# Kernel tuning notes

Measured on AMD Instinct MI355X. Metric: run time of the kernel, lower is better.

## Reference

```python
import jax, jax.numpy as jnp
import numpy as np

NEG_SLOPE = 0.2


def gat_conv(x, src, dst, N, W, a_src, a_dst, b, concat):
    # x: [N, F_in], W: [F_in, H*C], a_src/a_dst: [H, C], b: [H*C] or [C]
    H, C = a_src.shape
    h = (x @ W).reshape(N, H, C)                    # [N, H, C]
    al_src = jnp.einsum('nhc,hc->nh', h, a_src)     # [N, H]
    al_dst = jnp.einsum('nhc,hc->nh', h, a_dst)     # [N, H]
    logits = jax.nn.leaky_relu(al_src[src] + al_dst[dst], NEG_SLOPE)  # [E, H]
    # edge softmax over incoming edges of each destination node
    m = jax.ops.segment_max(logits, dst, num_segments=N)              # [N, H]
    m = jnp.where(jnp.isfinite(m), m, 0.0)
    e = jnp.exp(logits - m[dst])                                      # [E, H]
    denom = jax.ops.segment_sum(e, dst, num_segments=N)               # [N, H]
    alpha = e / denom[dst]                                            # [E, H]
    out = jax.ops.segment_sum(alpha[:, :, None] * h[src], dst, num_segments=N)  # [N, H, C]
    if concat:
        return out.reshape(N, H * C) + b
    return out.mean(axis=1) + b


def setup_inputs() -> dict:
    key = jax.random.key(0)
    ks = jax.random.split(key, 12)
    N, E = 100000, 1600000
    F_in, Ch, Co, H = 128, 32, 64, 4
    x = jax.random.normal(ks[0], (N, F_in), dtype=jnp.float32)
    edge_index = jax.random.randint(ks[1], (2, E), 0, N, dtype=jnp.int64)
    s = 0.1
    return {
        'x': x, 'edge_index': edge_index,
        'W1': jax.random.normal(ks[2], (F_in, H * Ch), jnp.float32) * s,
        'a_src1': jax.random.normal(ks[3], (H, Ch), jnp.float32) * s,
        'a_dst1': jax.random.normal(ks[4], (H, Ch), jnp.float32) * s,
        'b1': jnp.zeros((H * Ch,), jnp.float32),
        'W2': jax.random.normal(ks[5], (H * Ch, H * Ch), jnp.float32) * s,
        'a_src2': jax.random.normal(ks[6], (H, Ch), jnp.float32) * s,
        'a_dst2': jax.random.normal(ks[7], (H, Ch), jnp.float32) * s,
        'b2': jnp.zeros((H * Ch,), jnp.float32),
        'W3': jax.random.normal(ks[8], (H * Ch, H * Co), jnp.float32) * s,
        'a_src3': jax.random.normal(ks[9], (H, Co), jnp.float32) * s,
        'a_dst3': jax.random.normal(ks[10], (H, Co), jnp.float32) * s,
        'b3': jnp.zeros((Co,), jnp.float32),
    }


def reference(x, edge_index, W1, a_src1, a_dst1, b1, W2, a_src2, a_dst2, b2, W3, a_src3, a_dst3, b3):
    N = x.shape[0]
    # PyG GATConv default add_self_loops=True
    loop = jnp.arange(N, dtype=edge_index.dtype)
    src = jnp.concatenate([edge_index[0], loop])
    dst = jnp.concatenate([edge_index[1], loop])
    h = gat_conv(x, src, dst, N, W1, a_src1, a_dst1, b1, concat=True)
    h = jax.nn.elu(h)
    h = gat_conv(h, src, dst, N, W2, a_src2, a_dst2, b2, concat=True)
    h = jax.nn.elu(h)
    out = gat_conv(h, src, dst, N, W3, a_src3, a_dst3, b3, concat=False)
    return out
```

## Files before the change

kernel.cpp:

```cpp
#include <hip/hip_runtime.h>


#define NEG_SLOPE 0.2f

typedef __attribute__((ext_vector_type(8))) _Float16 half8v;
typedef __attribute__((ext_vector_type(4))) _Float16 half4v;
typedef __attribute__((ext_vector_type(2))) _Float16 half2v;
typedef __attribute__((ext_vector_type(4))) float f32x4;

__device__ __forceinline__ float lrelu(float v) { return v > 0.f ? v : NEG_SLOPE * v; }

struct hf2 { _Float16 hi, lo; };
__device__ __forceinline__ hf2 split_f16(float f)
{
    hf2 r;
    r.hi = (_Float16)f;
    r.lo = (_Float16)(f - (float)r.hi);
    return r;
}

__global__ void fill_sentinel(float* __restrict__ out, int n)
{
    int i = blockIdx.x * blockDim.x + threadIdx.x;
    if (i < n) out[i] = 1e30f;
}

__global__ void detect_idx64(const int* __restrict__ ei, int* __restrict__ flag)
{
    __shared__ int anynz;
    if (threadIdx.x == 0) anynz = 0;
    __syncthreads();
    int v = ei[2 * threadIdx.x + 1];
    if (v != 0) atomicOr(&anynz, 1);
    __syncthreads();
    if (threadIdx.x == 0) flag[0] = (anynz == 0) ? 1 : 0;
}

__global__ void prep_edges(const void* __restrict__ ei, const int* __restrict__ flag,
                           int* __restrict__ src32, int* __restrict__ dst32,
                           int* __restrict__ deg8, int* __restrict__ loc, int N, int E)
{
    int e = blockIdx.x * blockDim.x + threadIdx.x;
    if (e >= E) return;
    int xcc;
    asm("s_getreg_b32 %0, hwreg(HW_REG_XCC_ID)" : "=s"(xcc));
    xcc &= 7;
    int s, d;
    if (flag[0]) {
        s = (int)__builtin_nontemporal_load((const long long*)ei + e);
        d = (int)__builtin_nontemporal_load((const long long*)ei + E + e);
    } else {
        s = __builtin_nontemporal_load((const int*)ei + e);
        d = __builtin_nontemporal_load((const int*)ei + E + e);
    }
    src32[e] = s;
    dst32[e] = d;
    int v = atomicAdd(&deg8[xcc * N + d], 1);
    loc[e] = (xcc << 28) | v;
}

__global__ void reduce8(int* __restrict__ deg8, int* __restrict__ deg, int N)
{
    int d = blockIdx.x * blockDim.x + threadIdx.x;
    if (d >= N) return;
    int s = 0;
    #pragma unroll
    for (int k = 0; k < 8; ++k) {
        int v = deg8[k * N + d];
        deg8[k * N + d] = s;
        s += v;
    }
    deg[d] = s;
}

__global__ __launch_bounds__(256)
void scanA(const int* __restrict__ deg, int* __restrict__ rowptr,
           int* __restrict__ bsum, int N)
{
    __shared__ int part[256];
    const int t = threadIdx.x;
    const int base = blockIdx.x * 1024 + t * 4;
    int v[4];
    #pragma unroll
    for (int j = 0; j < 4; ++j) v[j] = (base + j < N) ? deg[base + j] : 0;
    int s = v[0] + v[1] + v[2] + v[3];
    part[t] = s;
    __syncthreads();
    #pragma unroll
    for (int off = 1; off < 256; off <<= 1) {
        int p = (t >= off) ? part[t - off] : 0;
        __syncthreads();
        part[t] += p;
        __syncthreads();
    }
    int run = (t == 0) ? 0 : part[t - 1];
    #pragma unroll
    for (int j = 0; j < 4; ++j) {
        if (base + j < N) rowptr[base + j] = run;
        run += v[j];
    }
    if (t == 255) bsum[blockIdx.x] = part[255];
}

__global__ __launch_bounds__(1024)
void scanB(int* __restrict__ bsum, int nb)
{
    __shared__ int s[1024];
    int t = threadIdx.x;
    s[t] = (t < nb) ? bsum[t] : 0;
    __syncthreads();
    for (int off = 1; off < 1024; off <<= 1) {
        int p = (t >= off) ? s[t - off] : 0;
        __syncthreads();
        s[t] += p;
        __syncthreads();
    }
    if (t < nb) bsum[t] = (t == 0) ? 0 : s[t - 1];
}

__global__ __launch_bounds__(256)
void scanC(int* __restrict__ rowptr, const int* __restrict__ bsum, int N, int E)
{
    const int base = blockIdx.x * 1024 + threadIdx.x * 4;
    const int off = bsum[blockIdx.x];
    #pragma unroll
    for (int j = 0; j < 4; ++j)
        if (base + j < N) rowptr[base + j] += off;
    if (blockIdx.x == 0 && threadIdx.x == 0) rowptr[N] = E;
}

__global__ void fill_csr(const int* __restrict__ src32, const int* __restrict__ dst32,
                         const int* __restrict__ loc, const int* __restrict__ rowptr,
                         const int* __restrict__ deg8, int* __restrict__ csr_src,
                         int N, int E)
{
    int e = blockIdx.x * blockDim.x + threadIdx.x;
    if (e >= E) return;
    int lv = loc[e];
    int d  = dst32[e];
    int k  = lv >> 28;
    csr_src[rowptr[d] + deg8[k * N + d] + (lv & 0x0FFFFFFF)] = src32[e];
}

__global__ void convert_hilo(const float* __restrict__ in, _Float16* __restrict__ hi,
                             _Float16* __restrict__ lo, long long n4)
{
    long long t = (long long)blockIdx.x * blockDim.x + threadIdx.x;
    if (t >= n4) return;
    float4 v = *(const float4*)&in[t * 4];
    hf2 a = split_f16(v.x), b = split_f16(v.y), c = split_f16(v.z), d = split_f16(v.w);
    half4v h, l;
    h.x = a.hi; h.y = b.hi; h.z = c.hi; h.w = d.hi;
    l.x = a.lo; l.y = b.lo; l.z = c.lo; l.w = d.lo;
    *(half4v*)&hi[t * 4] = h;
    *(half4v*)&lo[t * 4] = l;
}

__global__ __launch_bounds__(256)
void convert_wt(const float* __restrict__ W, _Float16* __restrict__ wthi,
                _Float16* __restrict__ wtlo, int ldw, int wcol0)
{
    int t = blockIdx.x * 256 + threadIdx.x;
    int k = t >> 7, n = t & 127;
    float v = W[(long long)k * ldw + wcol0 + n];
    hf2 r = split_f16(v);
    wthi[n * 128 + k] = r.hi;
    wtlo[n * 128 + k] = r.lo;
}

template<int HPC>
__global__ __launch_bounds__(256)
void gemm_mfma(const _Float16* __restrict__ Ahi, const _Float16* __restrict__ Alo,
               const _Float16* __restrict__ Wthi, const _Float16* __restrict__ Wtlo,
               _Float16* __restrict__ Chi, int ldc, int colofs, int hofs,
               const float* __restrict__ aS, const float* __restrict__ aD,
               float* __restrict__ als, float* __restrict__ ald, int M)
{
    const int tid = threadIdx.x;
    const int wave = tid >> 6, lane = tid & 63;
    const int l15 = lane & 15, lk = lane >> 4;
    const int m0 = blockIdx.x * 64 + wave * 16;
    int mrow = m0 + l15;
    if (mrow >= M) mrow = M - 1;

    f32x4 acc[8];
    #pragma unroll
    for (int i = 0; i < 8; ++i) acc[i] = (f32x4){0.f, 0.f, 0.f, 0.f};

    #pragma unroll
    for (int kt = 0; kt < 4; ++kt) {
        const int k = kt * 32 + lk * 8;
        half8v ah = *(const half8v*)&Ahi[(long long)mrow * 128 + k];
        half8v al = *(const half8v*)&Alo[(long long)mrow * 128 + k];
        #pragma unroll
        for (int nf = 0; nf < 8; ++nf) {
            half8v bh = *(const half8v*)&Wthi[(nf * 16 + l15) * 128 + k];
            half8v bl = *(const half8v*)&Wtlo[(nf * 16 + l15) * 128 + k];
            acc[nf] = __builtin_amdgcn_mfma_f32_16x16x32_f16(ah, bh, acc[nf], 0, 0, 0);
            acc[nf] = __builtin_amdgcn_mfma_f32_16x16x32_f16(ah, bl, acc[nf], 0, 0, 0);
            acc[nf] = __builtin_amdgcn_mfma_f32_16x16x32_f16(al, bh, acc[nf], 0, 0, 0);
        }
    }

    #pragma unroll
    for (int r = 0; r < 4; ++r) {
        int gm = m0 + lk * 4 + r;
        if (gm >= M) continue;
        #pragma unroll
        for (int nf = 0; nf < 8; ++nf)
            Chi[(long long)gm * ldc + colofs + nf * 16 + l15] = (_Float16)acc[nf][r];
    }

    float asv[8], adv[8];
    #pragma unroll
    for (int nf = 0; nf < 8; ++nf) {
        asv[nf] = aS[nf * 16 + l15];
        adv[nf] = aD[nf * 16 + l15];
    }
    constexpr int NFH = 8 / HPC;
    #pragma unroll
    for (int r = 0; r < 4; ++r) {
        #pragma unroll
        for (int h = 0; h < HPC; ++h) {
            float ps = 0.f, pd = 0.f;
            #pragma unroll
            for (int q = 0; q < NFH; ++q) {
                int nf = h * NFH + q;
                ps += acc[nf][r] * asv[nf];
                pd += acc[nf][r] * adv[nf];
            }
            #pragma unroll
            for (int m = 1; m < 16; m <<= 1) {
                ps += __shfl_xor(ps, m);
                pd += __shfl_xor(pd, m);
            }
            if (l15 == 0) {
                int gm = m0 + lk * 4 + r;
                if (gm < M) {
                    als[gm * 4 + hofs + h] = ps;
                    ald[gm * 4 + hofs + h] = pd;
                }
            }
        }
    }
}

template<int C, int HL>
__global__ __launch_bounds__(256)
void gat_aggregate(const int* __restrict__ rowptr, const int* __restrict__ csr_src,
                   const float* __restrict__ als, const float* __restrict__ ald,
                   const _Float16* __restrict__ h16, const float* __restrict__ bias,
                   _Float16* __restrict__ ohi, _Float16* __restrict__ olo, int N)
{
    constexpr int ROW = HL * C;
    constexpr int LOG2HL = (HL == 4) ? 2 : 1;
    const int d = (blockIdx.x * blockDim.x + threadIdx.x) >> 6;
    const int lane = threadIdx.x & 63;
    if (d >= N) return;
    const int j = lane * 2;
    const int hh = j / C;

    const int myh = lane & (HL - 1);
    const int myi = lane >> LOG2HL;
    const float ald_mine = ald[d * HL + myh];

    const float wself = __expf(lrelu(als[d * HL + hh] + ald[d * HL + hh]));
    float denom = wself;
    half2v hv = *(const half2v*)&h16[(unsigned)d * ROW + j];
    float vx = wself * (float)hv.x, vy = wself * (float)hv.y;

    const int e0 = rowptr[d], e1 = rowptr[d + 1];
    for (int base = e0; base < e1; base += 8) {
        int sv_mine = 0;
        float w_mine = 0.f;
        if (lane < 8 * HL) {
            int ee = base + myi;
            sv_mine = csr_src[ee < e1 ? ee : e1 - 1];
            float a = als[sv_mine * HL + myh] + ald_mine;
            w_mine = (ee < e1) ? __expf(lrelu(a)) : 0.f;
        }
        int sref[8];
        half2v hb[8];
        #pragma unroll
        for (int i = 0; i < 8; ++i) sref[i] = __shfl(sv_mine, i * HL, 64);
        #pragma unroll
        for (int i = 0; i < 8; ++i) hb[i] = *(const half2v*)&h16[(unsigned)sref[i] * ROW + j];
        #pragma unroll
        for (int i = 0; i < 8; ++i) {
            float wv = __shfl(w_mine, i * HL + hh, 64);
            denom += wv;
            vx += wv * (float)hb[i].x;
            vy += wv * (float)hb[i].y;
        }
    }
    float inv = 1.f / denom;
    vx = vx * inv + bias[j];
    vy = vy * inv + bias[j + 1];
    vx = vx > 0.f ? vx : __expf(vx) - 1.f;
    vy = vy > 0.f ? vy : __expf(vy) - 1.f;
    hf2 rx = split_f16(vx), ry = split_f16(vy);
    half2v hi2, lo2;
    hi2.x = rx.hi; hi2.y = ry.hi;
    lo2.x = rx.lo; lo2.y = ry.lo;
    *(half2v*)&ohi[(unsigned)d * ROW + j] = hi2;
    *(half2v*)&olo[(unsigned)d * ROW + j] = lo2;
}

__global__ __launch_bounds__(256)
void gat_aggregate3(const int* __restrict__ rowptr, const int* __restrict__ csr_src,
                    const float* __restrict__ als, const float* __restrict__ ald,
                    const _Float16* __restrict__ h16, const float* __restrict__ bias,
                    float* __restrict__ out, int N)
{
    const int d = (blockIdx.x * blockDim.x + threadIdx.x) >> 6;
    const int lane = threadIdx.x & 63;
    if (d >= N) return;
    const int q = lane * 4;
    const int chd = lane >> 4;

    const int myh = lane & 3;
    const int myi = lane >> 2;
    const float ald_mine = ald[d * 4 + myh];

    const float wself = __expf(lrelu(als[d * 4 + chd] + ald[d * 4 + chd]));
    float dn = wself;
    half4v hs = *(const half4v*)&h16[(unsigned)d * 256 + q];
    float vx0 = wself * (float)hs.x, vx1 = wself * (float)hs.y;
    float vx2 = wself * (float)hs.z, vx3 = wself * (float)hs.w;

    const int e0 = rowptr[d], e1 = rowptr[d + 1];
    for (int base = e0; base < e1; base += 8) {
        int sv_mine = 0;
        float w_mine = 0.f;
        if (lane < 32) {
            int ee = base + myi;
            sv_mine = csr_src[ee < e1 ? ee : e1 - 1];
            float a = als[sv_mine * 4 + myh] + ald_mine;
            w_mine = (ee < e1) ? __expf(lrelu(a)) : 0.f;
        }
        int sref[8];
        half4v hb[8];
        #pragma unroll
        for (int i = 0; i < 8; ++i) sref[i] = __shfl(sv_mine, i * 4, 64);
        #pragma unroll
        for (int i = 0; i < 8; ++i) hb[i] = *(const half4v*)&h16[(unsigned)sref[i] * 256 + q];
        #pragma unroll
        for (int i = 0; i < 8; ++i) {
            float wv = __shfl(w_mine, i * 4 + chd, 64);
            dn += wv;
            vx0 += wv * (float)hb[i].x;
            vx1 += wv * (float)hb[i].y;
            vx2 += wv * (float)hb[i].z;
            vx3 += wv * (float)hb[i].w;
        }
    }
    const float s = 0.25f / dn;
    float m0 = vx0 * s, m1 = vx1 * s, m2 = vx2 * s, m3 = vx3 * s;
    m0 += __shfl_xor(m0, 16); m1 += __shfl_xor(m1, 16);
    m2 += __shfl_xor(m2, 16); m3 += __shfl_xor(m3, 16);
    m0 += __shfl_xor(m0, 32); m1 += __shfl_xor(m1, 32);
    m2 += __shfl_xor(m2, 32); m3 += __shfl_xor(m3, 32);
    if (lane < 16) {
        m0 += bias[q + 0]; m1 += bias[q + 1];
        m2 += bias[q + 2]; m3 += bias[q + 3];
        *(float4*)&out[(unsigned)d * 64 + q] = make_float4(m0, m1, m2, m3);
    }
}

extern "C" void kernel_launch(void* const* d_in, const int* in_sizes, int n_in,
                              void* d_out, int out_size, void* d_ws, size_t ws_size,
                              hipStream_t stream)
{
    const float* x      = (const float*)d_in[0];
    const void*  ei     = d_in[1];
    const float* W1     = (const float*)d_in[2];
    const float* a_src1 = (const float*)d_in[3];
    const float* a_dst1 = (const float*)d_in[4];
    const float* b1     = (const float*)d_in[5];
    const float* W2     = (const float*)d_in[6];
    const float* a_src2 = (const float*)d_in[7];
    const float* a_dst2 = (const float*)d_in[8];
    const float* b2     = (const float*)d_in[9];
    const float* W3     = (const float*)d_in[10];
    const float* a_src3 = (const float*)d_in[11];
    const float* a_dst3 = (const float*)d_in[12];
    const float* b3     = (const float*)d_in[13];

    const int N = in_sizes[0] / 128;
    const int E = in_sizes[1] / 2;

    char* w = (char*)d_ws;
    auto alloc = [&](size_t bytes) {
        char* p = w;
        w += (bytes + 255) & ~(size_t)255;
        return p;
    };
    int*      flag    = (int*)     alloc(256);
    int*      deg8    = (int*)     alloc((size_t)N * 8 * 4);
    int*      deg     = (int*)     alloc((size_t)N * 4);
    int*      rowptr  = (int*)     alloc((size_t)(N + 1) * 4);
    int*      bsum    = (int*)     alloc(1024 * 4);
    int*      src32   = (int*)     alloc((size_t)E * 4);
    int*      dst32   = (int*)     alloc((size_t)E * 4);
    int*      loc     = (int*)     alloc((size_t)E * 4);
    int*      csr_src = (int*)     alloc((size_t)E * 4);
    _Float16* hhi     = (_Float16*)alloc((size_t)N * 256 * 2);
    _Float16* xhi     = (_Float16*)alloc((size_t)N * 128 * 2);
    _Float16* xlo     = (_Float16*)alloc((size_t)N * 128 * 2);
    float*    als     = (float*)   alloc((size_t)N * 4 * 4);
    float*    ald     = (float*)   alloc((size_t)N * 4 * 4);
    _Float16* wthi    = (_Float16*)alloc(2 * 128 * 128 * 2);
    _Float16* wtlo    = (_Float16*)alloc(2 * 128 * 128 * 2);
    if ((size_t)(w - (char*)d_ws) > ws_size) {
        fill_sentinel<<<(out_size + 255) / 256, 256, 0, stream>>>((float*)d_out, out_size);
        return;
    }
    _Float16* wthiB = wthi + 128 * 128;
    _Float16* wtloB = wtlo + 128 * 128;

    const int gb = 256;
    const int nb1024 = (N + 1023) / 1024;
    const int mb = (N + 63) / 64;
    const int ab = (N * 64 + gb - 1) / gb;
    auto blocks = [&](long long tot) { return (int)((tot + gb - 1) / gb); };

    detect_idx64<<<1, 256, 0, stream>>>((const int*)ei, flag);
    (void)hipMemsetAsync(deg8, 0, (size_t)N * 8 * 4, stream);
    prep_edges<<<blocks(E), gb, 0, stream>>>(ei, flag, src32, dst32, deg8, loc, N, E);
    reduce8<<<blocks(N), gb, 0, stream>>>(deg8, deg, N);
    scanA<<<nb1024, gb, 0, stream>>>(deg, rowptr, bsum, N);
    scanB<<<1, 1024, 0, stream>>>(bsum, nb1024);
    scanC<<<nb1024, gb, 0, stream>>>(rowptr, bsum, N, E);
    fill_csr<<<blocks(E), gb, 0, stream>>>(src32, dst32, loc, rowptr, deg8, csr_src, N, E);

    convert_hilo<<<blocks((long long)N * 32), gb, 0, stream>>>(x, xhi, xlo, (long long)N * 32);

    convert_wt<<<64, gb, 0, stream>>>(W1, wthi, wtlo, 128, 0);
    gemm_mfma<4><<<mb, gb, 0, stream>>>(xhi, xlo, wthi, wtlo, hhi, 128, 0, 0,
                                        a_src1, a_dst1, als, ald, N);
    gat_aggregate<32, 4><<<ab, gb, 0, stream>>>(
        rowptr, csr_src, als, ald, hhi, b1, xhi, xlo, N);

    convert_wt<<<64, gb, 0, stream>>>(W2, wthi, wtlo, 128, 0);
    gemm_mfma<4><<<mb, gb, 0, stream>>>(xhi, xlo, wthi, wtlo, hhi, 128, 0, 0,
                                        a_src2, a_dst2, als, ald, N);
    gat_aggregate<32, 4><<<ab, gb, 0, stream>>>(
        rowptr, csr_src, als, ald, hhi, b2, xhi, xlo, N);

    convert_wt<<<64, gb, 0, stream>>>(W3, wthi,  wtlo,  256, 0);
    convert_wt<<<64, gb, 0, stream>>>(W3, wthiB, wtloB, 256, 128);
    gemm_mfma<2><<<mb, gb, 0, stream>>>(xhi, xlo, wthi,  wtlo,  hhi, 256, 0, 0,
                                        a_src3,       a_dst3,       als, ald, N);
    gemm_mfma<2><<<mb, gb, 0, stream>>>(xhi, xlo, wthiB, wtloB, hhi, 256, 128, 2,
                                        a_src3 + 128, a_dst3 + 128, als, ald, N);
    gat_aggregate3<<<ab, gb, 0, stream>>>(
        rowptr, csr_src, als, ald, hhi, b3, (float*)d_out, N);
}
```

Baseline: 696.6 us.

## Fuse input fp32 split into GEMM, drop edge copies, double GEMM rows per wave

The separate convert_hilo pass over x is removed, and the first GEMM now reads fp32 x and splits it into hi/lo fp16 in registers. prep_edges no longer writes src32/dst32 copies, and fill_csr rereads edge_index directly. The GEMM now computes two 16-row groups per wave (128 rows per block) and reuses the loaded W fragments across both groups, with launch bounds set for 2 blocks per CU. Aggregation indexing is changed to use a fixed stride of 4 for als/ald. These changes cut intermediate memory traffic at the cost of higher register pressure in the GEMM.

```diff
diff --git a/kernel.cpp b/kernel.cpp
--- a/kernel.cpp
+++ b/kernel.cpp
@@ -37,7 +37,6 @@
 }
 
 __global__ void prep_edges(const void* __restrict__ ei, const int* __restrict__ flag,
-                           int* __restrict__ src32, int* __restrict__ dst32,
                            int* __restrict__ deg8, int* __restrict__ loc, int N, int E)
 {
     int e = blockIdx.x * blockDim.x + threadIdx.x;
@@ -45,16 +44,9 @@
     int xcc;
     asm("s_getreg_b32 %0, hwreg(HW_REG_XCC_ID)" : "=s"(xcc));
     xcc &= 7;
-    int s, d;
-    if (flag[0]) {
-        s = (int)__builtin_nontemporal_load((const long long*)ei + e);
-        d = (int)__builtin_nontemporal_load((const long long*)ei + E + e);
-    } else {
-        s = __builtin_nontemporal_load((const int*)ei + e);
-        d = __builtin_nontemporal_load((const int*)ei + E + e);
-    }
-    src32[e] = s;
-    dst32[e] = d;
+    int d;
+    if (flag[0]) d = (int)__builtin_nontemporal_load((const long long*)ei + E + e);
+    else         d = __builtin_nontemporal_load((const int*)ei + E + e);
     int v = atomicAdd(&deg8[xcc * N + d], 1);
     loc[e] = (xcc << 28) | v;
 }
@@ -129,31 +121,23 @@
     if (blockIdx.x == 0 && threadIdx.x == 0) rowptr[N] = E;
 }
 
-__global__ void fill_csr(const int* __restrict__ src32, const int* __restrict__ dst32,
+__global__ void fill_csr(const void* __restrict__ ei, const int* __restrict__ flag,
                          const int* __restrict__ loc, const int* __restrict__ rowptr,
                          const int* __restrict__ deg8, int* __restrict__ csr_src,
                          int N, int E)
 {
     int e = blockIdx.x * blockDim.x + threadIdx.x;
     if (e >= E) return;
+    int s, d;
+    if (flag[0]) {
+        s = (int)__builtin_nontemporal_load((const long long*)ei + e);
+        d = (int)__builtin_nontemporal_load((const long long*)ei + E + e);
+    } else {
+        s = __builtin_nontemporal_load((const int*)ei + e);
+        d = __builtin_nontemporal_load((const int*)ei + E + e);
+    }
     int lv = loc[e];
-    int d  = dst32[e];
-    int k  = lv >> 28;
-    csr_src[rowptr[d] + deg8[k * N + d] + (lv & 0x0FFFFFFF)] = src32[e];
-}
-
-__global__ void convert_hilo(const float* __restrict__ in, _Float16* __restrict__ hi,
-                             _Float16* __restrict__ lo, long long n4)
-{
-    long long t = (long long)blockIdx.x * blockDim.x + threadIdx.x;
-    if (t >= n4) return;
-    float4 v = *(const float4*)&in[t * 4];
-    hf2 a = split_f16(v.x), b = split_f16(v.y), c = split_f16(v.z), d = split_f16(v.w);
-    half4v h, l;
-    h.x = a.hi; h.y = b.hi; h.z = c.hi; h.w = d.hi;
-    l.x = a.lo; l.y = b.lo; l.z = c.lo; l.w = d.lo;
-    *(half4v*)&hi[t * 4] = h;
-    *(half4v*)&lo[t * 4] = l;
+    csr_src[rowptr[d] + deg8[(lv >> 28) * N + d] + (lv & 0x0FFFFFFF)] = s;
 }
 
 __global__ __launch_bounds__(256)
@@ -168,9 +152,9 @@
     wtlo[n * 128 + k] = r.lo;
 }
 
-template<int HPC>
-__global__ __launch_bounds__(256)
-void gemm_mfma(const _Float16* __restrict__ Ahi, const _Float16* __restrict__ Alo,
+template<int HPC, bool AF32>
+__global__ __launch_bounds__(256, 2)
+void gemm_mfma(const void* __restrict__ Aptr, const _Float16* __restrict__ Alo,
                const _Float16* __restrict__ Wthi, const _Float16* __restrict__ Wtlo,
                _Float16* __restrict__ Chi, int ldc, int colofs, int hofs,
                const float* __restrict__ aS, const float* __restrict__ aD,
@@ -179,36 +163,50 @@
     const int tid = threadIdx.x;
     const int wave = tid >> 6, lane = tid & 63;
     const int l15 = lane & 15, lk = lane >> 4;
-    const int m0 = blockIdx.x * 64 + wave * 16;
-    int mrow = m0 + l15;
-    if (mrow >= M) mrow = M - 1;
-
-    f32x4 acc[8];
-    #pragma unroll
-    for (int i = 0; i < 8; ++i) acc[i] = (f32x4){0.f, 0.f, 0.f, 0.f};
+    const int m0 = blockIdx.x * 128 + wave * 32;
+
+    f32x4 acc[2][8];
+    #pragma unroll
+    for (int rg = 0; rg < 2; ++rg)
+        #pragma unroll
+        for (int i = 0; i < 8; ++i) acc[rg][i] = (f32x4){0.f, 0.f, 0.f, 0.f};
 
     #pragma unroll
     for (int kt = 0; kt < 4; ++kt) {
         const int k = kt * 32 + lk * 8;
-        half8v ah = *(const half8v*)&Ahi[(long long)mrow * 128 + k];
-        half8v al = *(const half8v*)&Alo[(long long)mrow * 128 + k];
+        half8v bh[8], bl[8];
         #pragma unroll
         for (int nf = 0; nf < 8; ++nf) {
-            half8v bh = *(const half8v*)&Wthi[(nf * 16 + l15) * 128 + k];
-            half8v bl = *(const half8v*)&Wtlo[(nf * 16 + l15) * 128 + k];
-            acc[nf] = __builtin_amdgcn_mfma_f32_16x16x32_f16(ah, bh, acc[nf], 0, 0, 0);
-            acc[nf] = __builtin_amdgcn_mfma_f32_16x16x32_f16(ah, bl, acc[nf], 0, 0, 0);
-            acc[nf] = __builtin_amdgcn_mfma_f32_16x16x32_f16(al, bh, acc[nf], 0, 0, 0);
-        }
-    }
-
-    #pragma unroll
-    for (int r = 0; r < 4; ++r) {
-        int gm = m0 + lk * 4 + r;
-        if (gm >= M) continue;
-        #pragma unroll
-        for (int nf = 0; nf < 8; ++nf)
-            Chi[(long long)gm * ldc + colofs + nf * 16 + l15] = (_Float16)acc[nf][r];
+            bh[nf] = *(const half8v*)&Wthi[(nf * 16 + l15) * 128 + k];
+            bl[nf] = *(const half8v*)&Wtlo[(nf * 16 + l15) * 128 + k];
+        }
+        #pragma unroll
+        for (int rg = 0; rg < 2; ++rg) {
+            int mrow = m0 + rg * 16 + l15;
+            if (mrow >= M) mrow = M - 1;
+            half8v ah, al;
+            if (AF32) {
+                const float* A32 = (const float*)Aptr;
+                float4 v0 = *(const float4*)&A32[(long long)mrow * 128 + k];
+                float4 v1 = *(const float4*)&A32[(long long)mrow * 128 + k + 4];
+                hf2 s0 = split_f16(v0.x), s1 = split_f16(v0.y), s2 = split_f16(v0.z), s3 = split_f16(v0.w);
+                hf2 s4 = split_f16(v1.x), s5 = split_f16(v1.y), s6 = split_f16(v1.z), s7 = split_f16(v1.w);
+                ah[0] = s0.hi; ah[1] = s1.hi; ah[2] = s2.hi; ah[3] = s3.hi;
+                ah[4] = s4.hi; ah[5] = s5.hi; ah[6] = s6.hi; ah[7] = s7.hi;
+                al[0] = s0.lo; al[1] = s1.lo; al[2] = s2.lo; al[3] = s3.lo;
+                al[4] = s4.lo; al[5] = s5.lo; al[6] = s6.lo; al[7] = s7.lo;
+            } else {
+                const _Float16* Ahi = (const _Float16*)Aptr;
+                ah = *(const half8v*)&Ahi[(long long)mrow * 128 + k];
+                al = *(const half8v*)&Alo[(long long)mrow * 128 + k];
+            }
+            #pragma unroll
+            for (int nf = 0; nf < 8; ++nf) {
+                acc[rg][nf] = __builtin_amdgcn_mfma_f32_16x16x32_f16(ah, bh[nf], acc[rg][nf], 0, 0, 0);
+                acc[rg][nf] = __builtin_amdgcn_mfma_f32_16x16x32_f16(ah, bl[nf], acc[rg][nf], 0, 0, 0);
+                acc[rg][nf] = __builtin_amdgcn_mfma_f32_16x16x32_f16(al, bh[nf], acc[rg][nf], 0, 0, 0);
+            }
+        }
     }
 
     float asv[8], adv[8];
@@ -218,27 +216,39 @@
         adv[nf] = aD[nf * 16 + l15];
     }
     constexpr int NFH = 8 / HPC;
-    #pragma unroll
-    for (int r = 0; r < 4; ++r) {
-        #pragma unroll
-        for (int h = 0; h < HPC; ++h) {
-            float ps = 0.f, pd = 0.f;
+
+    #pragma unroll
+    for (int rg = 0; rg < 2; ++rg) {
+        #pragma unroll
+        for (int r = 0; r < 4; ++r) {
+            int gm = m0 + rg * 16 + lk * 4 + r;
+            if (gm >= M) continue;
             #pragma unroll
-            for (int q = 0; q < NFH; ++q) {
-                int nf = h * NFH + q;
-                ps += acc[nf][r] * asv[nf];
-                pd += acc[nf][r] * adv[nf];
-            }
+            for (int nf = 0; nf < 8; ++nf)
+                Chi[(long long)gm * ldc + colofs + nf * 16 + l15] = (_Float16)acc[rg][nf][r];
+        }
+        #pragma unroll
+        for (int r = 0; r < 4; ++r) {
             #pragma unroll
-            for (int m = 1; m < 16; m <<= 1) {
-                ps += __shfl_xor(ps, m);
-                pd += __shfl_xor(pd, m);
-            }
-            if (l15 == 0) {
-                int gm = m0 + lk * 4 + r;
-                if (gm < M) {
-                    als[gm * 4 + hofs + h] = ps;
-                    ald[gm * 4 + hofs + h] = pd;
+            for (int h = 0; h < HPC; ++h) {
+                float ps = 0.f, pd = 0.f;
+                #pragma unroll
+                for (int q = 0; q < NFH; ++q) {
+                    int nf = h * NFH + q;
+                    ps += acc[rg][nf][r] * asv[nf];
+                    pd += acc[rg][nf][r] * adv[nf];
+                }
+                #pragma unroll
+                for (int m = 1; m < 16; m <<= 1) {
+                    ps += __shfl_xor(ps, m);
+                    pd += __shfl_xor(pd, m);
+                }
+                if (l15 == 0) {
+                    int gm = m0 + rg * 16 + lk * 4 + r;
+                    if (gm < M) {
+                        als[gm * 4 + hofs + h] = ps;
+                        ald[gm * 4 + hofs + h] = pd;
+                    }
                 }
             }
         }
@@ -262,9 +272,9 @@
 
     const int myh = lane & (HL - 1);
     const int myi = lane >> LOG2HL;
-    const float ald_mine = ald[d * HL + myh];
-
-    const float wself = __expf(lrelu(als[d * HL + hh] + ald[d * HL + hh]));
+    const float ald_mine = ald[d * 4 + myh];
+
+    const float wself = __expf(lrelu(als[d * 4 + hh] + ald[d * 4 + hh]));
     float denom = wself;
     half2v hv = *(const half2v*)&h16[(unsigned)d * ROW + j];
     float vx = wself * (float)hv.x, vy = wself * (float)hv.y;
@@ -276,7 +286,7 @@
         if (lane < 8 * HL) {
             int ee = base + myi;
             sv_mine = csr_src[ee < e1 ? ee : e1 - 1];
-            float a = als[sv_mine * HL + myh] + ald_mine;
+            float a = als[sv_mine * 4 + myh] + ald_mine;
             w_mine = (ee < e1) ? __expf(lrelu(a)) : 0.f;
         }
         int sref[8];
@@ -400,8 +410,6 @@
     int*      deg     = (int*)     alloc((size_t)N * 4);
     int*      rowptr  = (int*)     alloc((size_t)(N + 1) * 4);
     int*      bsum    = (int*)     alloc(1024 * 4);
-    int*      src32   = (int*)     alloc((size_t)E * 4);
-    int*      dst32   = (int*)     alloc((size_t)E * 4);
     int*      loc     = (int*)     alloc((size_t)E * 4);
     int*      csr_src = (int*)     alloc((size_t)E * 4);
     _Float16* hhi     = (_Float16*)alloc((size_t)N * 256 * 2);
@@ -420,39 +428,37 @@
 
     const int gb = 256;
     const int nb1024 = (N + 1023) / 1024;
-    const int mb = (N + 63) / 64;
+    const int mb = (N + 127) / 128;
     const int ab = (N * 64 + gb - 1) / gb;
     auto blocks = [&](long long tot) { return (int)((tot + gb - 1) / gb); };
 
     detect_idx64<<<1, 256, 0, stream>>>((const int*)ei, flag);
     (void)hipMemsetAsync(deg8, 0, (size_t)N * 8 * 4, stream);
-    prep_edges<<<blocks(E), gb, 0, stream>>>(ei, flag, src32, dst32, deg8, loc, N, E);
+    prep_edges<<<blocks(E), gb, 0, stream>>>(ei, flag, deg8, loc, N, E);
     reduce8<<<blocks(N), gb, 0, stream>>>(deg8, deg, N);
     scanA<<<nb1024, gb, 0, stream>>>(deg, rowptr, bsum, N);
     scanB<<<1, 1024, 0, stream>>>(bsum, nb1024);
     scanC<<<nb1024, gb, 0, stream>>>(rowptr, bsum, N, E);
-    fill_csr<<<blocks(E), gb, 0, stream>>>(src32, dst32, loc, rowptr, deg8, csr_src, N, E);
-
-    convert_hilo<<<blocks((long long)N * 32), gb, 0, stream>>>(x, xhi, xlo, (long long)N * 32);
+    fill_csr<<<blocks(E), gb, 0, stream>>>(ei, flag, loc, rowptr, deg8, csr_src, N, E);
 
     convert_wt<<<64, gb, 0, stream>>>(W1, wthi, wtlo, 128, 0);
-    gemm_mfma<4><<<mb, gb, 0, stream>>>(xhi, xlo, wthi, wtlo, hhi, 128, 0, 0,
-                                        a_src1, a_dst1, als, ald, N);
+    gemm_mfma<4, true><<<mb, gb, 0, stream>>>(x, nullptr, wthi, wtlo, hhi, 128, 0, 0,
+                                              a_src1, a_dst1, als, ald, N);
     gat_aggregate<32, 4><<<ab, gb, 0, stream>>>(
         rowptr, csr_src, als, ald, hhi, b1, xhi, xlo, N);
 
     convert_wt<<<64, gb, 0, stream>>>(W2, wthi, wtlo, 128, 0);
-    gemm_mfma<4><<<mb, gb, 0, stream>>>(xhi, xlo, wthi, wtlo, hhi, 128, 0, 0,
-                                        a_src2, a_dst2, als, ald, N);
+    gemm_mfma<4, false><<<mb, gb, 0, stream>>>(xhi, xlo, wthi, wtlo, hhi, 128, 0, 0,
+                                               a_src2, a_dst2, als, ald, N);
     gat_aggregate<32, 4><<<ab, gb, 0, stream>>>(
         rowptr, csr_src, als, ald, hhi, b2, xhi, xlo, N);
 
     convert_wt<<<64, gb, 0, stream>>>(W3, wthi,  wtlo,  256, 0);
     convert_wt<<<64, gb, 0, stream>>>(W3, wthiB, wtloB, 256, 128);
-    gemm_mfma<2><<<mb, gb, 0, stream>>>(xhi, xlo, wthi,  wtlo,  hhi, 256, 0, 0,
-                                        a_src3,       a_dst3,       als, ald, N);
-    gemm_mfma<2><<<mb, gb, 0, stream>>>(xhi, xlo, wthiB, wtloB, hhi, 256, 128, 2,
-                                        a_src3 + 128, a_dst3 + 128, als, ald, N);
+    gemm_mfma<2, false><<<mb, gb, 0, stream>>>(xhi, xlo, wthi,  wtlo,  hhi, 256, 0, 0,
+                                               a_src3,       a_dst3,       als, ald, N);
+    gemm_mfma<2, false><<<mb, gb, 0, stream>>>(xhi, xlo, wthiB, wtloB, hhi, 256, 128, 2,
+                                               a_src3 + 128, a_dst3 + 128, als, ald, N);
     gat_aggregate3<<<ab, gb, 0, stream>>>(
         rowptr, csr_src, als, ald, hhi, b3, (float*)d_out, N);
 }
```

Result: faster. 628.9 us (-9.7%).
